# Kernel optimization log

Measured on AMD Instinct MI355X. Metric: run time of the kernel, lower is better.

Reference implementation:

```python
import jax, jax.numpy as jnp
import numpy as np

B = 32768
NM = 3      # number of modalities (len(mk))
NE = 8      # number of experts
D_IN = 768
D_P = 128   # per-modality projection dim
D_X = D_P * NM  # 384, concatenated feature dim


def setup_inputs() -> dict:
    key = jax.random.key(0)
    ks = jax.random.split(key, 16)
    s = 0.02
    return {
        "feat_text": jax.random.normal(ks[0], (B, D_IN), jnp.float32),
        "feat_audio": jax.random.normal(ks[1], (B, D_IN), jnp.float32),
        "feat_video": jax.random.normal(ks[2], (B, D_IN), jnp.float32),
        "proj_w": jax.random.normal(ks[3], (NM, D_IN, D_P), jnp.float32) * s,
        "proj_b": jax.random.normal(ks[4], (NM, D_P), jnp.float32) * s,
        "exp_w1": jax.random.normal(ks[5], (NE, D_X, D_P), jnp.float32) * s,
        "exp_b1": jax.random.normal(ks[6], (NE, D_P), jnp.float32) * s,
        "exp_w2": jax.random.normal(ks[7], (NE, D_P, D_P), jnp.float32) * s,
        "exp_b2": jax.random.normal(ks[8], (NE, D_P), jnp.float32) * s,
        "gate_w": jax.random.normal(ks[9], (D_X, NE), jnp.float32) * s,
        "gate_b": jax.random.normal(ks[10], (NE,), jnp.float32) * s,
        "pre_w": jax.random.normal(ks[11], (D_P, 64), jnp.float32) * s,
        "pre_b": jax.random.normal(ks[12], (64,), jnp.float32) * s,
        "head_w": jax.random.normal(ks[13], (64, 2), jnp.float32) * s,
        "head_b": jax.random.normal(ks[14], (2,), jnp.float32) * s,
    }


def reference(feat_text, feat_audio, feat_video, proj_w, proj_b,
              exp_w1, exp_b1, exp_w2, exp_b2, gate_w, gate_b,
              pre_w, pre_b, head_w, head_b):
    feats = jnp.stack([feat_text, feat_audio, feat_video], axis=0)  # [M,B,768]
    # per-modality projections, then concat: [B, 128*M]
    proj = jnp.einsum('mbd,mdp->mbp', feats, proj_w) + proj_b[:, None, :]
    x = jnp.concatenate(jnp.split(proj, NM, axis=0), axis=-1)[0]  # [B, 384]
    # gate: softmax over 8 experts
    gw = jax.nn.softmax(x @ gate_w + gate_b, axis=-1)  # [B, 8]
    # all experts as batched GEMM: [E,B,128]
    h = jax.nn.relu(jnp.einsum('bx,exh->ebh', x, exp_w1) + exp_b1[:, None, :])
    eo = jnp.einsum('ebh,eho->ebo', h, exp_w2) + exp_b2[:, None, :]
    fused = jnp.einsum('be,ebh->bh', gw, eo)  # weighted sum over experts
    penult = jax.nn.relu(fused @ pre_w + pre_b)  # Dropout is identity in eval
    logits = penult @ head_w + head_b  # [B, 2]
    return logits
```

## Files before the change

### kernel.cpp

```cpp
#include <hip/hip_runtime.h>
#include <hip/hip_bf16.h>

#define B_ROWS 32768

typedef unsigned short u16;
typedef unsigned int u32;
typedef float f32x4 __attribute__((ext_vector_type(4)));
typedef __bf16 bf16x8 __attribute__((ext_vector_type(8)));

__device__ __forceinline__ u16 f2bf(float f){
    union { float f; u32 u; } v; v.f = f;
    return (u16)((v.u + 0x7FFFu + ((v.u >> 16) & 1u)) >> 16);
}
__device__ __forceinline__ float bf2f(u16 h){
    union { u32 u; float f; } v; v.u = ((u32)h) << 16; return v.f;
}
__device__ __forceinline__ u32 cvtpk(float lo, float hi){
    u32 r;
    asm("v_cvt_pk_bf16_f32 %0, %1, %2" : "=v"(r) : "v"(lo), "v"(hi));
    return r;
}
__device__ __forceinline__ void async_cp16(void* lds_dst, const void* g_src){
    __builtin_amdgcn_global_load_lds(
        (const __attribute__((address_space(1))) unsigned int*)g_src,
        (__attribute__((address_space(3))) unsigned int*)lds_dst, 16, 0, 0);
}

__global__ void cast_weights_kernel(const float* __restrict__ proj_w,
                                    const float* __restrict__ exp_w1,
                                    const float* __restrict__ exp_w2,
                                    const float* __restrict__ pre_w,
                                    const float* __restrict__ gate_w,
                                    u16* __restrict__ pimg, u16* __restrict__ w1img,
                                    u16* __restrict__ w2img, u16* __restrict__ prwT,
                                    u16* __restrict__ gwimg){
    int i = blockIdx.x * 256 + threadIdx.x;
    if (i < 294912){
        int m = i / 98304, r = i % 98304;
        int c = r / 4096, rr = r % 4096;
        int col = rr >> 5, kk = rr & 31;
        int kb = kk ^ (((col >> 1) & 3) << 3);
        pimg[i] = f2bf(proj_w[m*98304 + (c*32 + kb)*128 + col]);
    } else if (i < 688128){
        int j = i - 294912;
        int e = j / 49152, r = j % 49152;
        int ph = r / 4096, rr = r % 4096;
        int q = rr >> 10, col = (rr >> 3) & 127, el = rr & 7;
        w1img[j] = f2bf(exp_w1[e*49152 + (ph*32 + q*8 + el)*128 + col]);
    } else if (i < 819200){
        int j = i - 688128;
        int e = j / 16384, r = j % 16384;
        int c2 = r / 4096, rr = r % 4096;
        int q = rr >> 10, col = (rr >> 3) & 127, el = rr & 7;
        w2img[j] = f2bf(exp_w2[e*16384 + (c2*32 + q*8 + el)*128 + col]);
    } else if (i < 827392){
        int j = i - 819200;
        int o = j / 128, k = j % 128;
        prwT[j] = f2bf(pre_w[k*64 + o]);
    } else if (i < 833536){
        int j = i - 827392;
        int e = j / 384, k = j % 384;
        gwimg[j] = (e < 8) ? f2bf(gate_w[k*8 + e]) : (u16)0;
    }
}

#define XS_OFF   0
#define A_OFF    98304
#define B_OFF    147456
#define HS_OFF   98304
#define GWT_OFF  131072
#define B1_OFF   135168
#define B2_OFF   137216
#define WB_OFF   139264

__global__ __launch_bounds__(512, 2) void fused_kernel(
    const float* __restrict__ ft, const float* __restrict__ fa, const float* __restrict__ fv,
    const u16* __restrict__ pimg, const float* __restrict__ proj_b,
    const u16* __restrict__ w1img, const u16* __restrict__ w2img,
    const u16* __restrict__ prwT, const u16* __restrict__ gwimg,
    const float* __restrict__ gate_b, const float* __restrict__ exp_b1, const float* __restrict__ exp_b2,
    const float* __restrict__ pre_b, const float* __restrict__ head_w, const float* __restrict__ head_b,
    float* __restrict__ out)
{
    __shared__ __align__(16) char lds[163840];
    const int tid = threadIdx.x;
    const int lane = tid & 63, wid = tid >> 6;
    const int wr = wid >> 1, wc = wid & 1;
    const int lr = lane & 15, q = lane >> 4;
    const int blk = blockIdx.x;
    const int row0 = blk * 128;
    const char* w1b = (const char*)w1img;
    const char* w2b = (const char*)w2img;
    char* HsB = lds + HS_OFF;
    u16* b1L = (u16*)(lds + B1_OFF);
    u16* b2L = (u16*)(lds + B2_OFF);

    float pb0[4], pb1[4], pb2[4];
    #pragma unroll
    for (int ni = 0; ni < 4; ni++){
        int c = wc*64 + ni*16 + lr;
        pb0[ni] = proj_b[c];
        pb1[ni] = proj_b[128 + c];
        pb2[ni] = proj_b[256 + c];
    }
    asm volatile("s_waitcnt vmcnt(0)" ::: "memory");

    u32 aoffs[2];
    #pragma unroll
    for (int i = 0; i < 2; i++){
        int P = i*8192 + tid*16;
        int row = P >> 7, inner = P & 127;
        aoffs[i] = (u32)((row0 + row)*3072 + (inner ^ ((row & 7) << 4)));
    }

#define ASTAGE(c) do{                                                          \
        int mm_ = (c) / 24, kk_ = (c) % 24;                                    \
        const char* ab_ = (const char*)(mm_ == 0 ? ft : mm_ == 1 ? fa : fv);   \
        char* la_ = lds + A_OFF + ((c) % 3)*16384 + tid*16;                    \
        async_cp16(la_,        ab_ + aoffs[0] + kk_*128);                      \
        async_cp16(la_ + 8192, ab_ + aoffs[1] + kk_*128);                      \
    }while(0)

#define BSTAGE(c) do{                                                          \
        int mm_ = (c) / 24, kk_ = (c) % 24;                                    \
        async_cp16(lds + B_OFF + ((c) % 2)*8192 + tid*16,                      \
                   (const char*)pimg + mm_*196608 + kk_*8192 + tid*16);        \
    }while(0)

#define PCONSUME(c) do{                                                        \
        const char* Abuf = lds + A_OFF + ((c) % 3)*16384;                      \
        const char* Bbuf = lds + B_OFF + ((c) % 2)*8192;                       \
        bf16x8 af[2];                                                          \
        _Pragma("unroll")                                                      \
        for (int mi = 0; mi < 2; mi++){                                        \
            int row = wr*32 + mi*16 + lr;                                      \
            int aoff = row*128 + ((q*32) ^ ((row & 7) << 4));                  \
            f32x4 a0 = *(const f32x4*)(Abuf + aoff);                           \
            f32x4 a1 = *(const f32x4*)(Abuf + (aoff ^ 16));                    \
            union { u32 w[4]; bf16x8 v; } u;                                   \
            u.w[0] = cvtpk(a0.x, a0.y); u.w[1] = cvtpk(a0.z, a0.w);            \
            u.w[2] = cvtpk(a1.x, a1.y); u.w[3] = cvtpk(a1.z, a1.w);            \
            af[mi] = u.v;                                                      \
        }                                                                      \
        _Pragma("unroll")                                                      \
        for (int ni = 0; ni < 4; ni++){                                        \
            int col = wc*64 + ni*16 + lr;                                      \
            int boff = col*64 + ((q*16) ^ (((col >> 1) & 3) << 4));            \
            bf16x8 bf = *(const bf16x8*)(Bbuf + boff);                         \
            acc[0][ni] = __builtin_amdgcn_mfma_f32_16x16x32_bf16(af[0], bf, acc[0][ni], 0, 0, 0); \
            acc[1][ni] = __builtin_amdgcn_mfma_f32_16x16x32_bf16(af[1], bf, acc[1][ni], 0, 0, 0); \
        }                                                                      \
    }while(0)

#define PHASE_A_MOD(MC, PB) do{                                                \
        _Pragma("unroll 1")                                                    \
        for (int kt = 0; kt < 24; kt++){                                       \
            int t = MC*24 + kt;                                                \
            __builtin_amdgcn_sched_barrier(0);                                 \
            __builtin_amdgcn_s_barrier();                                      \
            if (t < 71) BSTAGE(t + 1);                                         \
            if (t < 70) ASTAGE(t + 2);                                         \
            if (t < 70)       asm volatile("s_waitcnt vmcnt(5)" ::: "memory"); \
            else if (t == 70) asm volatile("s_waitcnt vmcnt(3)" ::: "memory"); \
            else              asm volatile("s_waitcnt vmcnt(0)" ::: "memory"); \
            __builtin_amdgcn_s_barrier();                                      \
            __builtin_amdgcn_sched_barrier(0);                                 \
            PCONSUME(t);                                                       \
        }                                                                      \
        _Pragma("unroll")                                                      \
        for (int mi = 0; mi < 2; mi++)                                         \
            _Pragma("unroll")                                                  \
            for (int ni = 0; ni < 4; ni++){                                    \
                int lcol = wc*64 + ni*16 + lr;                                 \
                int colg = MC*128 + lcol;                                      \
                int ktI = colg >> 5, qI = (colg >> 3) & 3, el = colg & 7;      \
                _Pragma("unroll")                                              \
                for (int j = 0; j < 4; j++){                                   \
                    int row = wr*32 + mi*16 + q*4 + j;                         \
                    *(u16*)(lds + (row >> 6)*49152 + ktI*4096 + qI*1024        \
                            + (row & 63)*16 + el*2) = f2bf(acc[mi][ni][j] + PB[ni]); \
                    acc[mi][ni][j] = 0.f;                                      \
                }                                                              \
            }                                                                  \
    }while(0)

    f32x4 acc[2][4];
    #pragma unroll
    for (int i = 0; i < 2; i++)
        #pragma unroll
        for (int j = 0; j < 4; j++) acc[i][j] = {0.f, 0.f, 0.f, 0.f};

    BSTAGE(0); ASTAGE(0); ASTAGE(1);
    PHASE_A_MOD(0, pb0);
    PHASE_A_MOD(1, pb1);
    PHASE_A_MOD(2, pb2);
#undef ASTAGE
#undef BSTAGE
#undef PCONSUME
#undef PHASE_A_MOD

    asm volatile("s_waitcnt lgkmcnt(0)" ::: "memory");
    __builtin_amdgcn_sched_barrier(0);
    __builtin_amdgcn_s_barrier();

    async_cp16(lds + WB_OFF + 0*8192 + tid*16, w1b + tid*16);
    async_cp16(lds + WB_OFF + 1*8192 + tid*16, w1b + 8192 + tid*16);
    for (int i = tid; i < 1024; i += 512){
        b1L[i] = f2bf(exp_b1[i]);
        b2L[i] = f2bf(exp_b2[i]);
    }
    {
        f32x4 ga = {0.f, 0.f, 0.f, 0.f};
        const char* xb = lds + (wid >> 2)*49152 + ((wid & 3)*16 + lr)*16 + q*1024;
        const u16* gwp = gwimg + lr*384 + q*8;
        #pragma unroll
        for (int kt = 0; kt < 12; kt++){
            bf16x8 af = *(const bf16x8*)(xb + kt*4096);
            bf16x8 gb = *(const bf16x8*)(gwp + kt*32);
            ga = __builtin_amdgcn_mfma_f32_16x16x32_bf16(af, gb, ga, 0, 0, 0);
        }
        float gbv = gate_b[lr & 7];
        float gw4[4];
        #pragma unroll
        for (int j = 0; j < 4; j++){
            float v = ga[j] + gbv;
            float mx = v;
            mx = fmaxf(mx, __shfl_xor(mx, 1));
            mx = fmaxf(mx, __shfl_xor(mx, 2));
            mx = fmaxf(mx, __shfl_xor(mx, 4));
            float s = __expf(v - mx);
            float t = s;
            t += __shfl_xor(t, 1);
            t += __shfl_xor(t, 2);
            t += __shfl_xor(t, 4);
            gw4[j] = s / t;
        }
        if (lr < 8){
            f32x4 wv = {gw4[0], gw4[1], gw4[2], gw4[3]};
            *(f32x4*)(lds + GWT_OFF + lr*512 + (wid*16 + q*4)*4) = wv;
        }
    }
    asm volatile("s_waitcnt vmcnt(0) lgkmcnt(0)" ::: "memory");
    __builtin_amdgcn_sched_barrier(0);
    __builtin_amdgcn_s_barrier();

#define WSTAGE(g) do{                                                          \
        int gn_ = (g) > 127 ? 127 : (g);                                       \
        int en_ = gn_ >> 4, pn_ = gn_ & 15;                                    \
        const char* src_ = (pn_ < 12) ? (w1b + en_*98304 + pn_*8192)           \
                                      : (w2b + en_*32768 + (pn_ - 12)*8192);   \
        async_cp16(lds + WB_OFF + ((g) % 3)*8192 + tid*16, src_ + tid*16);     \
    }while(0)

    f32x4 fus[2][4];
    #pragma unroll
    for (int i = 0; i < 2; i++)
        #pragma unroll
        for (int j = 0; j < 4; j++) fus[i][j] = {0.f, 0.f, 0.f, 0.f};

    #pragma unroll 1
    for (int e = 0; e < 8; e++){
        f32x4 ac1[2][4];
        #pragma unroll
        for (int i = 0; i < 2; i++)
            #pragma unroll
            for (int j = 0; j < 4; j++) ac1[i][j] = {0.f, 0.f, 0.f, 0.f};

        #pragma unroll 1
        for (int ph = 0; ph < 12; ph++){
            int g = e*16 + ph;
            __builtin_amdgcn_sched_barrier(0);
            __builtin_amdgcn_s_barrier();
            WSTAGE(g + 2);
            asm volatile("s_waitcnt vmcnt(2)" ::: "memory");
            __builtin_amdgcn_s_barrier();
            __builtin_amdgcn_sched_barrier(0);
            const char* wsl = lds + WB_OFF + (g % 3)*8192 + q*2048;
            const char* xa  = lds + (wr >> 1)*49152 + ph*4096 + q*1024;
            bf16x8 af0 = *(const bf16x8*)(xa + ((wr & 1)*32 + lr)*16);
            bf16x8 af1 = *(const bf16x8*)(xa + ((wr & 1)*32 + 16 + lr)*16);
            #pragma unroll
            for (int ni = 0; ni < 4; ni++){
                bf16x8 bf = *(const bf16x8*)(wsl + (wc*64 + ni*16 + lr)*16);
                ac1[0][ni] = __builtin_amdgcn_mfma_f32_16x16x32_bf16(af0, bf, ac1[0][ni], 0, 0, 0);
                ac1[1][ni] = __builtin_amdgcn_mfma_f32_16x16x32_bf16(af1, bf, ac1[1][ni], 0, 0, 0);
            }
        }
        #pragma unroll
        for (int mi = 0; mi < 2; mi++)
            #pragma unroll
            for (int ni = 0; ni < 4; ni++){
                int col = wc*64 + ni*16 + lr;
                float b1v = bf2f(b1L[e*128 + col]);
                #pragma unroll
                for (int j = 0; j < 4; j++){
                    int row = wr*32 + mi*16 + q*4 + j;
                    *(u16*)(HsB + row*256 + ((col*2) ^ ((row & 7) << 4)))
                        = f2bf(fmaxf(ac1[mi][ni][j] + b1v, 0.f));
                }
            }
        asm volatile("s_waitcnt lgkmcnt(0)" ::: "memory");
        __builtin_amdgcn_sched_barrier(0);

        f32x4 ac2[2][4];
        #pragma unroll
        for (int i = 0; i < 2; i++)
            #pragma unroll
            for (int j = 0; j < 4; j++) ac2[i][j] = {0.f, 0.f, 0.f, 0.f};

        #pragma unroll 1
        for (int p2 = 0; p2 < 4; p2++){
            int g = e*16 + 12 + p2;
            __builtin_amdgcn_sched_barrier(0);
            __builtin_amdgcn_s_barrier();
            WSTAGE(g + 2);
            asm volatile("s_waitcnt vmcnt(2)" ::: "memory");
            __builtin_amdgcn_s_barrier();
            __builtin_amdgcn_sched_barrier(0);
            const char* wsl = lds + WB_OFF + (g % 3)*8192 + q*2048;
            int cb = p2*64 + q*16;
            int rowA = wr*32 + lr;
            int rowB = wr*32 + 16 + lr;
            bf16x8 af0 = *(const bf16x8*)(HsB + rowA*256 + (cb ^ ((rowA & 7) << 4)));
            bf16x8 af1 = *(const bf16x8*)(HsB + rowB*256 + (cb ^ ((rowB & 7) << 4)));
            #pragma unroll
            for (int ni = 0; ni < 4; ni++){
                bf16x8 bf = *(const bf16x8*)(wsl + (wc*64 + ni*16 + lr)*16);
                ac2[0][ni] = __builtin_amdgcn_mfma_f32_16x16x32_bf16(af0, bf, ac2[0][ni], 0, 0, 0);
                ac2[1][ni] = __builtin_amdgcn_mfma_f32_16x16x32_bf16(af1, bf, ac2[1][ni], 0, 0, 0);
            }
        }
        #pragma unroll
        for (int mi = 0; mi < 2; mi++){
            f32x4 gwv = *(const f32x4*)(lds + GWT_OFF + e*512 + (wr*32 + mi*16 + q*4)*4);
            #pragma unroll
            for (int ni = 0; ni < 4; ni++){
                int col = wc*64 + ni*16 + lr;
                float b2v = bf2f(b2L[e*128 + col]);
                #pragma unroll
                for (int j = 0; j < 4; j++)
                    fus[mi][ni][j] += gwv[j] * (ac2[mi][ni][j] + b2v);
            }
        }
    }
#undef WSTAGE

    asm volatile("s_waitcnt vmcnt(0)" ::: "memory");
    __builtin_amdgcn_sched_barrier(0);
    __builtin_amdgcn_s_barrier();
    #pragma unroll
    for (int mi = 0; mi < 2; mi++)
        #pragma unroll
        for (int ni = 0; ni < 4; ni++){
            int col = wc*64 + ni*16 + lr;
            #pragma unroll
            for (int j = 0; j < 4; j++){
                int row = wr*32 + mi*16 + q*4 + j;
                *(u16*)(HsB + row*256 + ((col*2) ^ ((row & 7) << 4))) = f2bf(fus[mi][ni][j]);
            }
        }
    asm volatile("s_waitcnt lgkmcnt(0)" ::: "memory");
    __builtin_amdgcn_sched_barrier(0);
    __builtin_amdgcn_s_barrier();

    f32x4 ap[4];
    #pragma unroll
    for (int i = 0; i < 4; i++) ap[i] = {0.f, 0.f, 0.f, 0.f};
    #pragma unroll
    for (int kt = 0; kt < 4; kt++){
        int row = wid*16 + lr;
        int cb = kt*64 + q*16;
        bf16x8 af = *(const bf16x8*)(HsB + row*256 + (cb ^ ((row & 7) << 4)));
        #pragma unroll
        for (int ni = 0; ni < 4; ni++){
            bf16x8 bf = *(const bf16x8*)(prwT + (size_t)(ni*16 + lr)*128 + kt*32 + q*8);
            ap[ni] = __builtin_amdgcn_mfma_f32_16x16x32_bf16(af, bf, ap[ni], 0, 0, 0);
        }
    }
    float* Pen = (float*)lds;
    #pragma unroll
    for (int ni = 0; ni < 4; ni++){
        int col = ni*16 + lr;
        float pbv = pre_b[col];
        #pragma unroll
        for (int j = 0; j < 4; j++){
            int row = wid*16 + q*4 + j;
            Pen[row*68 + col] = fmaxf(ap[ni][j] + pbv, 0.f);
        }
    }
    asm volatile("s_waitcnt lgkmcnt(0)" ::: "memory");
    __builtin_amdgcn_sched_barrier(0);
    __builtin_amdgcn_s_barrier();
    if (tid < 256){
        int r = tid >> 1, c = tid & 1;
        float s = head_b[c];
        #pragma unroll 8
        for (int k = 0; k < 64; k++) s += Pen[r*68 + k] * head_w[k*2 + c];
        out[(size_t)(blk*128 + r)*2 + c] = s;
    }
}

extern "C" void kernel_launch(void* const* d_in, const int* in_sizes, int n_in,
                              void* d_out, int out_size, void* d_ws, size_t ws_size,
                              hipStream_t stream) {
    const float* ft     = (const float*)d_in[0];
    const float* fa     = (const float*)d_in[1];
    const float* fv     = (const float*)d_in[2];
    const float* proj_w = (const float*)d_in[3];
    const float* proj_b = (const float*)d_in[4];
    const float* exp_w1 = (const float*)d_in[5];
    const float* exp_b1 = (const float*)d_in[6];
    const float* exp_w2 = (const float*)d_in[7];
    const float* exp_b2 = (const float*)d_in[8];
    const float* gate_w = (const float*)d_in[9];
    const float* gate_b = (const float*)d_in[10];
    const float* pre_w  = (const float*)d_in[11];
    const float* pre_b  = (const float*)d_in[12];
    const float* head_w = (const float*)d_in[13];
    const float* head_b = (const float*)d_in[14];
    float* out = (float*)d_out;

    u16* pimg  = (u16*)d_ws;
    u16* w1img = pimg + 294912;
    u16* w2img = w1img + 393216;
    u16* prwT  = w2img + 131072;
    u16* gwimg = prwT + 8192;

    cast_weights_kernel<<<3256, 256, 0, stream>>>(proj_w, exp_w1, exp_w2, pre_w, gate_w,
                                                  pimg, w1img, w2img, prwT, gwimg);
    fused_kernel<<<256, 512, 0, stream>>>(ft, fa, fv, pimg, proj_b,
                                          w1img, w2img, prwT, gwimg,
                                          gate_b, exp_b1, exp_b2,
                                          pre_b, head_w, head_b, out);
}
```

Before: 121.0 us.

## Halve block tile to 64 rows with 256 threads and double-buffered pipelines

Shrinks each block from 128 to 64 rows and from 512 to 256 threads, halving LDS to 80KB so two blocks fit per CU, and launches 512 blocks so every CU gets work on a 256-CU part. The projection pipeline moves from triple-buffered A with prefetch depth two to double buffering with depth one. The expert weight stream becomes single-buffered, with each load issued after compute and waited on immediately. That trades latency hiding inside a block for more resident blocks and better grid fill.

```diff
diff --git a/kernel.cpp b/kernel.cpp
--- a/kernel.cpp
+++ b/kernel.cpp
@@ -65,15 +65,15 @@
 }
 
 #define XS_OFF   0
-#define A_OFF    98304
-#define B_OFF    147456
-#define HS_OFF   98304
-#define GWT_OFF  131072
-#define B1_OFF   135168
-#define B2_OFF   137216
-#define WB_OFF   139264
-
-__global__ __launch_bounds__(512, 2) void fused_kernel(
+#define A_OFF    49152
+#define B_OFF    65536
+#define HS_OFF   49152
+#define GWT_OFF  65536
+#define B1_OFF   67584
+#define B2_OFF   69632
+#define WB_OFF   71680
+
+__global__ __launch_bounds__(256, 2) void fused_kernel(
     const float* __restrict__ ft, const float* __restrict__ fa, const float* __restrict__ fv,
     const u16* __restrict__ pimg, const float* __restrict__ proj_b,
     const u16* __restrict__ w1img, const u16* __restrict__ w2img,
@@ -82,13 +82,13 @@
     const float* __restrict__ pre_b, const float* __restrict__ head_w, const float* __restrict__ head_b,
     float* __restrict__ out)
 {
-    __shared__ __align__(16) char lds[163840];
+    __shared__ __align__(16) char lds[81920];
     const int tid = threadIdx.x;
     const int lane = tid & 63, wid = tid >> 6;
     const int wr = wid >> 1, wc = wid & 1;
     const int lr = lane & 15, q = lane >> 4;
     const int blk = blockIdx.x;
-    const int row0 = blk * 128;
+    const int row0 = blk * 64;
     const char* w1b = (const char*)w1img;
     const char* w2b = (const char*)w2img;
     char* HsB = lds + HS_OFF;
@@ -108,7 +108,7 @@
     u32 aoffs[2];
     #pragma unroll
     for (int i = 0; i < 2; i++){
-        int P = i*8192 + tid*16;
+        int P = i*4096 + tid*16;
         int row = P >> 7, inner = P & 127;
         aoffs[i] = (u32)((row0 + row)*3072 + (inner ^ ((row & 7) << 4)));
     }
@@ -116,20 +116,22 @@
 #define ASTAGE(c) do{                                                          \
         int mm_ = (c) / 24, kk_ = (c) % 24;                                    \
         const char* ab_ = (const char*)(mm_ == 0 ? ft : mm_ == 1 ? fa : fv);   \
-        char* la_ = lds + A_OFF + ((c) % 3)*16384 + tid*16;                    \
+        char* la_ = lds + A_OFF + ((c) & 1)*8192 + tid*16;                     \
         async_cp16(la_,        ab_ + aoffs[0] + kk_*128);                      \
-        async_cp16(la_ + 8192, ab_ + aoffs[1] + kk_*128);                      \
+        async_cp16(la_ + 4096, ab_ + aoffs[1] + kk_*128);                      \
     }while(0)
 
 #define BSTAGE(c) do{                                                          \
         int mm_ = (c) / 24, kk_ = (c) % 24;                                    \
-        async_cp16(lds + B_OFF + ((c) % 2)*8192 + tid*16,                      \
-                   (const char*)pimg + mm_*196608 + kk_*8192 + tid*16);        \
+        const char* gb_ = (const char*)pimg + mm_*196608 + kk_*8192 + tid*16;  \
+        char* lb_ = lds + B_OFF + ((c) & 1)*8192 + tid*16;                     \
+        async_cp16(lb_,        gb_);                                           \
+        async_cp16(lb_ + 4096, gb_ + 4096);                                    \
     }while(0)
 
 #define PCONSUME(c) do{                                                        \
-        const char* Abuf = lds + A_OFF + ((c) % 3)*16384;                      \
-        const char* Bbuf = lds + B_OFF + ((c) % 2)*8192;                       \
+        const char* Abuf = lds + A_OFF + ((c) & 1)*8192;                       \
+        const char* Bbuf = lds + B_OFF + ((c) & 1)*8192;                       \
         bf16x8 af[2];                                                          \
         _Pragma("unroll")                                                      \
         for (int mi = 0; mi < 2; mi++){                                        \
@@ -158,11 +160,12 @@
             int t = MC*24 + kt;                                                \
             __builtin_amdgcn_sched_barrier(0);                                 \
             __builtin_amdgcn_s_barrier();                                      \
-            if (t < 71) BSTAGE(t + 1);                                         \
-            if (t < 70) ASTAGE(t + 2);                                         \
-            if (t < 70)       asm volatile("s_waitcnt vmcnt(5)" ::: "memory"); \
-            else if (t == 70) asm volatile("s_waitcnt vmcnt(3)" ::: "memory"); \
-            else              asm volatile("s_waitcnt vmcnt(0)" ::: "memory"); \
+            if (t < 71){                                                       \
+                ASTAGE(t + 1); BSTAGE(t + 1);                                  \
+                asm volatile("s_waitcnt vmcnt(4)" ::: "memory");               \
+            } else {                                                           \
+                asm volatile("s_waitcnt vmcnt(0)" ::: "memory");               \
+            }                                                                  \
             __builtin_amdgcn_s_barrier();                                      \
             __builtin_amdgcn_sched_barrier(0);                                 \
             PCONSUME(t);                                                       \
@@ -177,8 +180,8 @@
                 _Pragma("unroll")                                              \
                 for (int j = 0; j < 4; j++){                                   \
                     int row = wr*32 + mi*16 + q*4 + j;                         \
-                    *(u16*)(lds + (row >> 6)*49152 + ktI*4096 + qI*1024        \
-                            + (row & 63)*16 + el*2) = f2bf(acc[mi][ni][j] + PB[ni]); \
+                    *(u16*)(lds + ktI*4096 + qI*1024 + row*16 + el*2)          \
+                        = f2bf(acc[mi][ni][j] + PB[ni]);                       \
                     acc[mi][ni][j] = 0.f;                                      \
                 }                                                              \
             }                                                                  \
@@ -190,7 +193,7 @@
         #pragma unroll
         for (int j = 0; j < 4; j++) acc[i][j] = {0.f, 0.f, 0.f, 0.f};
 
-    BSTAGE(0); ASTAGE(0); ASTAGE(1);
+    ASTAGE(0); BSTAGE(0);
     PHASE_A_MOD(0, pb0);
     PHASE_A_MOD(1, pb1);
     PHASE_A_MOD(2, pb2);
@@ -203,15 +206,15 @@
     __builtin_amdgcn_sched_barrier(0);
     __builtin_amdgcn_s_barrier();
 
-    async_cp16(lds + WB_OFF + 0*8192 + tid*16, w1b + tid*16);
-    async_cp16(lds + WB_OFF + 1*8192 + tid*16, w1b + 8192 + tid*16);
-    for (int i = tid; i < 1024; i += 512){
+    async_cp16(lds + WB_OFF + tid*16,        w1b + tid*16);
+    async_cp16(lds + WB_OFF + tid*16 + 4096, w1b + tid*16 + 4096);
+    for (int i = tid; i < 1024; i += 256){
         b1L[i] = f2bf(exp_b1[i]);
         b2L[i] = f2bf(exp_b2[i]);
     }
     {
         f32x4 ga = {0.f, 0.f, 0.f, 0.f};
-        const char* xb = lds + (wid >> 2)*49152 + ((wid & 3)*16 + lr)*16 + q*1024;
+        const char* xb = lds + (wid*16 + lr)*16 + q*1024;
         const u16* gwp = gwimg + lr*384 + q*8;
         #pragma unroll
         for (int kt = 0; kt < 12; kt++){
@@ -237,7 +240,7 @@
         }
         if (lr < 8){
             f32x4 wv = {gw4[0], gw4[1], gw4[2], gw4[3]};
-            *(f32x4*)(lds + GWT_OFF + lr*512 + (wid*16 + q*4)*4) = wv;
+            *(f32x4*)(lds + GWT_OFF + lr*256 + (wid*16 + q*4)*4) = wv;
         }
     }
     asm volatile("s_waitcnt vmcnt(0) lgkmcnt(0)" ::: "memory");
@@ -245,11 +248,11 @@
     __builtin_amdgcn_s_barrier();
 
 #define WSTAGE(g) do{                                                          \
-        int gn_ = (g) > 127 ? 127 : (g);                                       \
-        int en_ = gn_ >> 4, pn_ = gn_ & 15;                                    \
+        int en_ = (g) >> 4, pn_ = (g) & 15;                                    \
         const char* src_ = (pn_ < 12) ? (w1b + en_*98304 + pn_*8192)           \
                                       : (w2b + en_*32768 + (pn_ - 12)*8192);   \
-        async_cp16(lds + WB_OFF + ((g) % 3)*8192 + tid*16, src_ + tid*16);     \
+        async_cp16(lds + WB_OFF + tid*16,        src_ + tid*16);               \
+        async_cp16(lds + WB_OFF + tid*16 + 4096, src_ + tid*16 + 4096);        \
     }while(0)
 
     f32x4 fus[2][4];
@@ -269,22 +272,21 @@
         #pragma unroll 1
         for (int ph = 0; ph < 12; ph++){
             int g = e*16 + ph;
-            __builtin_amdgcn_sched_barrier(0);
-            __builtin_amdgcn_s_barrier();
-            WSTAGE(g + 2);
-            asm volatile("s_waitcnt vmcnt(2)" ::: "memory");
-            __builtin_amdgcn_s_barrier();
-            __builtin_amdgcn_sched_barrier(0);
-            const char* wsl = lds + WB_OFF + (g % 3)*8192 + q*2048;
-            const char* xa  = lds + (wr >> 1)*49152 + ph*4096 + q*1024;
-            bf16x8 af0 = *(const bf16x8*)(xa + ((wr & 1)*32 + lr)*16);
-            bf16x8 af1 = *(const bf16x8*)(xa + ((wr & 1)*32 + 16 + lr)*16);
+            const char* wsl = lds + WB_OFF + q*2048;
+            bf16x8 af0 = *(const bf16x8*)(lds + ph*4096 + q*1024 + (wr*32 + lr)*16);
+            bf16x8 af1 = *(const bf16x8*)(lds + ph*4096 + q*1024 + (wr*32 + 16 + lr)*16);
             #pragma unroll
             for (int ni = 0; ni < 4; ni++){
                 bf16x8 bf = *(const bf16x8*)(wsl + (wc*64 + ni*16 + lr)*16);
                 ac1[0][ni] = __builtin_amdgcn_mfma_f32_16x16x32_bf16(af0, bf, ac1[0][ni], 0, 0, 0);
                 ac1[1][ni] = __builtin_amdgcn_mfma_f32_16x16x32_bf16(af1, bf, ac1[1][ni], 0, 0, 0);
             }
+            __builtin_amdgcn_sched_barrier(0);
+            __builtin_amdgcn_s_barrier();
+            WSTAGE(g + 1);
+            asm volatile("s_waitcnt vmcnt(0)" ::: "memory");
+            __builtin_amdgcn_s_barrier();
+            __builtin_amdgcn_sched_barrier(0);
         }
         #pragma unroll
         for (int mi = 0; mi < 2; mi++)
@@ -301,6 +303,7 @@
             }
         asm volatile("s_waitcnt lgkmcnt(0)" ::: "memory");
         __builtin_amdgcn_sched_barrier(0);
+        __builtin_amdgcn_s_barrier();
 
         f32x4 ac2[2][4];
         #pragma unroll
@@ -311,13 +314,7 @@
         #pragma unroll 1
         for (int p2 = 0; p2 < 4; p2++){
             int g = e*16 + 12 + p2;
-            __builtin_amdgcn_sched_barrier(0);
-            __builtin_amdgcn_s_barrier();
-            WSTAGE(g + 2);
-            asm volatile("s_waitcnt vmcnt(2)" ::: "memory");
-            __builtin_amdgcn_s_barrier();
-            __builtin_amdgcn_sched_barrier(0);
-            const char* wsl = lds + WB_OFF + (g % 3)*8192 + q*2048;
+            const char* wsl = lds + WB_OFF + q*2048;
             int cb = p2*64 + q*16;
             int rowA = wr*32 + lr;
             int rowB = wr*32 + 16 + lr;
@@ -329,10 +326,18 @@
                 ac2[0][ni] = __builtin_amdgcn_mfma_f32_16x16x32_bf16(af0, bf, ac2[0][ni], 0, 0, 0);
                 ac2[1][ni] = __builtin_amdgcn_mfma_f32_16x16x32_bf16(af1, bf, ac2[1][ni], 0, 0, 0);
             }
+            __builtin_amdgcn_sched_barrier(0);
+            __builtin_amdgcn_s_barrier();
+            if (g < 127){
+                WSTAGE(g + 1);
+                asm volatile("s_waitcnt vmcnt(0)" ::: "memory");
+            }
+            __builtin_amdgcn_s_barrier();
+            __builtin_amdgcn_sched_barrier(0);
         }
         #pragma unroll
         for (int mi = 0; mi < 2; mi++){
-            f32x4 gwv = *(const f32x4*)(lds + GWT_OFF + e*512 + (wr*32 + mi*16 + q*4)*4);
+            f32x4 gwv = *(const f32x4*)(lds + GWT_OFF + e*256 + (wr*32 + mi*16 + q*4)*4);
             #pragma unroll
             for (int ni = 0; ni < 4; ni++){
                 int col = wc*64 + ni*16 + lr;
@@ -345,7 +350,6 @@
     }
 #undef WSTAGE
 
-    asm volatile("s_waitcnt vmcnt(0)" ::: "memory");
     __builtin_amdgcn_sched_barrier(0);
     __builtin_amdgcn_s_barrier();
     #pragma unroll
@@ -391,12 +395,12 @@
     asm volatile("s_waitcnt lgkmcnt(0)" ::: "memory");
     __builtin_amdgcn_sched_barrier(0);
     __builtin_amdgcn_s_barrier();
-    if (tid < 256){
+    if (tid < 128){
         int r = tid >> 1, c = tid & 1;
         float s = head_b[c];
         #pragma unroll 8
         for (int k = 0; k < 64; k++) s += Pen[r*68 + k] * head_w[k*2 + c];
-        out[(size_t)(blk*128 + r)*2 + c] = s;
+        out[(size_t)(blk*64 + r)*2 + c] = s;
     }
 }
 
@@ -428,7 +432,7 @@
 
     cast_weights_kernel<<<3256, 256, 0, stream>>>(proj_w, exp_w1, exp_w2, pre_w, gate_w,
                                                   pimg, w1img, w2img, prwT, gwimg);
-    fused_kernel<<<256, 512, 0, stream>>>(ft, fa, fv, pimg, proj_b,
+    fused_kernel<<<512, 256, 0, stream>>>(ft, fa, fv, pimg, proj_b,
                                           w1img, w2img, prwT, gwimg,
                                           gate_b, exp_b1, exp_b2,
                                           pre_b, head_w, head_b, out);
```

New measurement: 142.2 us. +17.5%, slower.

## Stage expert weights in multi-slice groups to cut per-slice barriers

Applied to the files above, without the earlier changes.

Replaces the per-slice 3-deep ring prefetch of expert weights with group staging: three W1 slices or two W2 slices are loaded at once, consumed, then the next group is loaded into the same slots. This cuts the number of block barriers and waitcnt points per expert from 16 to 6. In exchange the next group's global-to-LDS load is waited on immediately, so load latency is no longer overlapped with MFMA compute.

```diff
diff --git a/kernel.cpp b/kernel.cpp
--- a/kernel.cpp
+++ b/kernel.cpp
@@ -203,8 +203,12 @@
     __builtin_amdgcn_sched_barrier(0);
     __builtin_amdgcn_s_barrier();
 
-    async_cp16(lds + WB_OFF + 0*8192 + tid*16, w1b + tid*16);
-    async_cp16(lds + WB_OFF + 1*8192 + tid*16, w1b + 8192 + tid*16);
+    {
+        const char* src = w1b + tid*16;
+        async_cp16(lds + WB_OFF + 0*8192 + tid*16, src);
+        async_cp16(lds + WB_OFF + 1*8192 + tid*16, src + 8192);
+        async_cp16(lds + WB_OFF + 2*8192 + tid*16, src + 16384);
+    }
     for (int i = tid; i < 1024; i += 512){
         b1L[i] = f2bf(exp_b1[i]);
         b2L[i] = f2bf(exp_b2[i]);
@@ -244,12 +248,18 @@
     __builtin_amdgcn_sched_barrier(0);
     __builtin_amdgcn_s_barrier();
 
-#define WSTAGE(g) do{                                                          \
-        int gn_ = (g) > 127 ? 127 : (g);                                       \
-        int en_ = gn_ >> 4, pn_ = gn_ & 15;                                    \
-        const char* src_ = (pn_ < 12) ? (w1b + en_*98304 + pn_*8192)           \
-                                      : (w2b + en_*32768 + (pn_ - 12)*8192);   \
-        async_cp16(lds + WB_OFF + ((g) % 3)*8192 + tid*16, src_ + tid*16);     \
+#define WGROUP_STAGE(gg2) do{                                                  \
+        int e2_ = (gg2) / 6, i2_ = (gg2) % 6;                                  \
+        if (i2_ < 4){                                                          \
+            const char* src_ = w1b + e2_*98304 + i2_*3*8192 + tid*16;          \
+            async_cp16(lds + WB_OFF + 0*8192 + tid*16, src_);                  \
+            async_cp16(lds + WB_OFF + 1*8192 + tid*16, src_ + 8192);           \
+            async_cp16(lds + WB_OFF + 2*8192 + tid*16, src_ + 16384);          \
+        } else {                                                               \
+            const char* src_ = w2b + e2_*32768 + (i2_ - 4)*2*8192 + tid*16;    \
+            async_cp16(lds + WB_OFF + 0*8192 + tid*16, src_);                  \
+            async_cp16(lds + WB_OFF + 1*8192 + tid*16, src_ + 8192);           \
+        }                                                                      \
     }while(0)
 
     f32x4 fus[2][4];
@@ -267,68 +277,78 @@
             for (int j = 0; j < 4; j++) ac1[i][j] = {0.f, 0.f, 0.f, 0.f};
 
         #pragma unroll 1
-        for (int ph = 0; ph < 12; ph++){
-            int g = e*16 + ph;
+        for (int grp = 0; grp < 4; grp++){
+            #pragma unroll
+            for (int c = 0; c < 3; c++){
+                int ph = grp*3 + c;
+                const char* wsl = lds + WB_OFF + c*8192 + q*2048;
+                const char* xa  = lds + (wr >> 1)*49152 + ph*4096 + q*1024;
+                bf16x8 af0 = *(const bf16x8*)(xa + ((wr & 1)*32 + lr)*16);
+                bf16x8 af1 = *(const bf16x8*)(xa + ((wr & 1)*32 + 16 + lr)*16);
+                #pragma unroll
+                for (int ni = 0; ni < 4; ni++){
+                    bf16x8 bf = *(const bf16x8*)(wsl + (wc*64 + ni*16 + lr)*16);
+                    ac1[0][ni] = __builtin_amdgcn_mfma_f32_16x16x32_bf16(af0, bf, ac1[0][ni], 0, 0, 0);
+                    ac1[1][ni] = __builtin_amdgcn_mfma_f32_16x16x32_bf16(af1, bf, ac1[1][ni], 0, 0, 0);
+                }
+            }
+            if (grp == 3){
+                #pragma unroll
+                for (int mi = 0; mi < 2; mi++)
+                    #pragma unroll
+                    for (int ni = 0; ni < 4; ni++){
+                        int col = wc*64 + ni*16 + lr;
+                        float b1v = bf2f(b1L[e*128 + col]);
+                        #pragma unroll
+                        for (int j = 0; j < 4; j++){
+                            int row = wr*32 + mi*16 + q*4 + j;
+                            *(u16*)(HsB + row*256 + ((col*2) ^ ((row & 7) << 4)))
+                                = f2bf(fmaxf(ac1[mi][ni][j] + b1v, 0.f));
+                        }
+                    }
+                asm volatile("s_waitcnt lgkmcnt(0)" ::: "memory");
+            }
             __builtin_amdgcn_sched_barrier(0);
             __builtin_amdgcn_s_barrier();
-            WSTAGE(g + 2);
-            asm volatile("s_waitcnt vmcnt(2)" ::: "memory");
+            WGROUP_STAGE(e*6 + grp + 1);
+            asm volatile("s_waitcnt vmcnt(0)" ::: "memory");
             __builtin_amdgcn_s_barrier();
             __builtin_amdgcn_sched_barrier(0);
-            const char* wsl = lds + WB_OFF + (g % 3)*8192 + q*2048;
-            const char* xa  = lds + (wr >> 1)*49152 + ph*4096 + q*1024;
-            bf16x8 af0 = *(const bf16x8*)(xa + ((wr & 1)*32 + lr)*16);
-            bf16x8 af1 = *(const bf16x8*)(xa + ((wr & 1)*32 + 16 + lr)*16);
-            #pragma unroll
-            for (int ni = 0; ni < 4; ni++){
-                bf16x8 bf = *(const bf16x8*)(wsl + (wc*64 + ni*16 + lr)*16);
-                ac1[0][ni] = __builtin_amdgcn_mfma_f32_16x16x32_bf16(af0, bf, ac1[0][ni], 0, 0, 0);
-                ac1[1][ni] = __builtin_amdgcn_mfma_f32_16x16x32_bf16(af1, bf, ac1[1][ni], 0, 0, 0);
-            }
-        }
-        #pragma unroll
-        for (int mi = 0; mi < 2; mi++)
-            #pragma unroll
-            for (int ni = 0; ni < 4; ni++){
-                int col = wc*64 + ni*16 + lr;
-                float b1v = bf2f(b1L[e*128 + col]);
+        }
+
+        f32x4 ac2[2][4];
+        #pragma unroll
+        for (int i = 0; i < 2; i++)
+            #pragma unroll
+            for (int j = 0; j < 4; j++) ac2[i][j] = {0.f, 0.f, 0.f, 0.f};
+
+        #pragma unroll 1
+        for (int grp = 0; grp < 2; grp++){
+            #pragma unroll
+            for (int c = 0; c < 2; c++){
+                int p2 = grp*2 + c;
+                const char* wsl = lds + WB_OFF + c*8192 + q*2048;
+                int cb = p2*64 + q*16;
+                int rowA = wr*32 + lr;
+                int rowB = wr*32 + 16 + lr;
+                bf16x8 af0 = *(const bf16x8*)(HsB + rowA*256 + (cb ^ ((rowA & 7) << 4)));
+                bf16x8 af1 = *(const bf16x8*)(HsB + rowB*256 + (cb ^ ((rowB & 7) << 4)));
                 #pragma unroll
-                for (int j = 0; j < 4; j++){
-                    int row = wr*32 + mi*16 + q*4 + j;
-                    *(u16*)(HsB + row*256 + ((col*2) ^ ((row & 7) << 4)))
-                        = f2bf(fmaxf(ac1[mi][ni][j] + b1v, 0.f));
+                for (int ni = 0; ni < 4; ni++){
+                    bf16x8 bf = *(const bf16x8*)(wsl + (wc*64 + ni*16 + lr)*16);
+                    ac2[0][ni] = __builtin_amdgcn_mfma_f32_16x16x32_bf16(af0, bf, ac2[0][ni], 0, 0, 0);
+                    ac2[1][ni] = __builtin_amdgcn_mfma_f32_16x16x32_bf16(af1, bf, ac2[1][ni], 0, 0, 0);
                 }
             }
-        asm volatile("s_waitcnt lgkmcnt(0)" ::: "memory");
-        __builtin_amdgcn_sched_barrier(0);
-
-        f32x4 ac2[2][4];
-        #pragma unroll
-        for (int i = 0; i < 2; i++)
-            #pragma unroll
-            for (int j = 0; j < 4; j++) ac2[i][j] = {0.f, 0.f, 0.f, 0.f};
-
-        #pragma unroll 1
-        for (int p2 = 0; p2 < 4; p2++){
-            int g = e*16 + 12 + p2;
+            int gg2 = e*6 + 5 + grp;
             __builtin_amdgcn_sched_barrier(0);
             __builtin_amdgcn_s_barrier();
-            WSTAGE(g + 2);
-            asm volatile("s_waitcnt vmcnt(2)" ::: "memory");
+            if (gg2 < 48){
+                WGROUP_STAGE(gg2);
+                asm volatile("s_waitcnt vmcnt(0)" ::: "memory");
+            }
             __builtin_amdgcn_s_barrier();
             __builtin_amdgcn_sched_barrier(0);
-            const char* wsl = lds + WB_OFF + (g % 3)*8192 + q*2048;
-            int cb = p2*64 + q*16;
-            int rowA = wr*32 + lr;
-            int rowB = wr*32 + 16 + lr;
-            bf16x8 af0 = *(const bf16x8*)(HsB + rowA*256 + (cb ^ ((rowA & 7) << 4)));
-            bf16x8 af1 = *(const bf16x8*)(HsB + rowB*256 + (cb ^ ((rowB & 7) << 4)));
-            #pragma unroll
-            for (int ni = 0; ni < 4; ni++){
-                bf16x8 bf = *(const bf16x8*)(wsl + (wc*64 + ni*16 + lr)*16);
-                ac2[0][ni] = __builtin_amdgcn_mfma_f32_16x16x32_bf16(af0, bf, ac2[0][ni], 0, 0, 0);
-                ac2[1][ni] = __builtin_amdgcn_mfma_f32_16x16x32_bf16(af1, bf, ac2[1][ni], 0, 0, 0);
-            }
         }
         #pragma unroll
         for (int mi = 0; mi < 2; mi++){
@@ -343,9 +363,8 @@
             }
         }
     }
-#undef WSTAGE
-
-    asm volatile("s_waitcnt vmcnt(0)" ::: "memory");
+#undef WGROUP_STAGE
+
     __builtin_amdgcn_sched_barrier(0);
     __builtin_amdgcn_s_barrier();
     #pragma unroll
```

New measurement: 120.9 us. Within noise of the previous version (-0.1%).
